# Performance work log

Hardware: AMD Instinct MI355X
Metric: run time of the kernel (lower is better)

Reference implementation:

```python
import jax, jax.numpy as jnp
import numpy as np

EPS = 1e-4  # LayerNorm epsilon from module


def layer_norm(x):
    # torch: (x - mean) / (std + eps), std unbiased (ddof=1), no affine
    mean = jnp.mean(x, axis=-1, keepdims=True)
    std = jnp.sqrt(jnp.var(x, axis=-1, ddof=1, keepdims=True))
    return (x - mean) / (std + EPS)


def setup_inputs() -> dict:
    key = jax.random.key(0)
    ks = jax.random.split(key, 9)
    B, S, D, H, QK = 2, 2048, 1024, 16, 64
    E = D // H  # per-head value/output dim
    scale = 0.02
    x = jax.random.normal(ks[0], (B, S, D), dtype=jnp.float32)
    # stacked per-head projection weights, Linear as x @ W + b
    Wq = jax.random.normal(ks[1], (H, D, QK), dtype=jnp.float32) * scale
    bq = jax.random.normal(ks[2], (H, QK), dtype=jnp.float32) * scale
    Wk = jax.random.normal(ks[3], (H, D, QK), dtype=jnp.float32) * scale
    bk = jax.random.normal(ks[4], (H, QK), dtype=jnp.float32) * scale
    Wv = jax.random.normal(ks[5], (H, D, E), dtype=jnp.float32) * scale
    bv = jax.random.normal(ks[6], (H, E), dtype=jnp.float32) * scale
    Wff = jax.random.normal(ks[7], (D, D), dtype=jnp.float32) * scale
    bff = jax.random.normal(ks[8], (D,), dtype=jnp.float32) * scale
    return {"x": x, "Wq": Wq, "bq": bq, "Wk": Wk, "bk": bk,
            "Wv": Wv, "bv": bv, "Wff": Wff, "bff": bff}


def reference(x, Wq, bq, Wk, bk, Wv, bv, Wff, bff):
    B, S, D = x.shape
    # all heads at once (vectorized over the Python per-head loop)
    Q = jnp.einsum('bsd,hdq->bhsq', x, Wq) + bq[None, :, None, :]
    K = jnp.einsum('bsd,hdq->bhsq', x, Wk) + bk[None, :, None, :]
    V = jnp.einsum('bsd,hde->bhse', x, Wv) + bv[None, :, None, :]
    scores = jnp.einsum('bhsq,bhtq->bhst', Q, K)  # [B,H,S,S]
    # masked_fill on tril(..., diagonal=-1): strictly-lower entries -> -inf
    mask = jnp.tril(jnp.ones((S, S), dtype=bool), k=-1)
    scores = jnp.where(mask[None, None], -jnp.inf, scores)
    # non-standard softmax axis: dim=-2 (over rows s, not keys t)
    attn = jax.nn.softmax(scores, axis=-2)
    heads = jnp.einsum('bhst,bhte->bhse', attn, V)  # [B,H,S,E]
    H, E = heads.shape[1], heads.shape[3]
    combined = heads.transpose(0, 2, 1, 3).reshape(B, S, H * E)  # concat heads
    x = layer_norm(x + combined)
    x = x + (x @ Wff + bff)
    return layer_norm(x)
```

## Files before the change

### kernel.cpp

```cpp
#include <hip/hip_runtime.h>
#include <hip/hip_bf16.h>
#include <math.h>

typedef unsigned short u16;
typedef __attribute__((ext_vector_type(8))) short short8;
typedef __attribute__((ext_vector_type(4))) short short4v;
typedef __attribute__((ext_vector_type(4))) float f32x4;

constexpr int B  = 2;
constexpr int S  = 2048;
constexpr int D  = 1024;
constexpr int H  = 16;
constexpr int DK = 64;
constexpr int BS = B * S;

__device__ __forceinline__ u16 f2b(float f) {
    __hip_bfloat16 h = __float2bfloat16(f);
    return *reinterpret_cast<u16*>(&h);
}
__device__ __forceinline__ float b2f(short s) {
    unsigned int u = ((unsigned int)(u16)s) << 16;
    return __builtin_bit_cast(float, u);
}

#define MFMA16(a, b, c) __builtin_amdgcn_mfma_f32_16x16x32_bf16((a), (b), (c), 0, 0, 0)

__global__ __launch_bounds__(256) void convert_x(const float* __restrict__ src,
                                                 u16* __restrict__ dst)
{
    size_t i = ((size_t)blockIdx.x * 256 + threadIdx.x) * 8;
    f32x4 a = *reinterpret_cast<const f32x4*>(src + i);
    f32x4 b = *reinterpret_cast<const f32x4*>(src + i + 4);
    short8 o;
    o[0] = (short)f2b(a[0]); o[1] = (short)f2b(a[1]);
    o[2] = (short)f2b(a[2]); o[3] = (short)f2b(a[3]);
    o[4] = (short)f2b(b[0]); o[5] = (short)f2b(b[1]);
    o[6] = (short)f2b(b[2]); o[7] = (short)f2b(b[3]);
    *reinterpret_cast<short8*>(dst + i) = o;
}

__global__ __launch_bounds__(256) void tconv(const float* __restrict__ src,
                                             u16* __restrict__ dst, int R, int C)
{
    const int bb = blockIdx.z;
    src += (size_t)bb * R * C;
    dst += (size_t)bb * R * C;
    const int c0 = blockIdx.x * 64, r0 = blockIdx.y * 64;
    __shared__ float Ts[64][65];
    const int tid = threadIdx.x;
    #pragma unroll
    for (int i = 0; i < 4; ++i) {
        int idx = i * 1024 + tid * 4;
        int r = idx >> 6, c = idx & 63;
        f32x4 v = *reinterpret_cast<const f32x4*>(&src[(size_t)(r0 + r) * C + c0 + c]);
        Ts[r][c] = v[0]; Ts[r][c + 1] = v[1]; Ts[r][c + 2] = v[2]; Ts[r][c + 3] = v[3];
    }
    __syncthreads();
    #pragma unroll
    for (int i = 0; i < 4; ++i) {
        int cc = i * 16 + (tid >> 4);
        int rr = (tid & 15) * 4;
        short4v pk;
        pk[0] = (short)f2b(Ts[rr][cc]);     pk[1] = (short)f2b(Ts[rr + 1][cc]);
        pk[2] = (short)f2b(Ts[rr + 2][cc]); pk[3] = (short)f2b(Ts[rr + 3][cc]);
        *reinterpret_cast<short4v*>(&dst[(size_t)(c0 + cc) * R + r0 + rr]) = pk;
    }
}

__global__ __launch_bounds__(256) void qkv_gemm(
    const u16* __restrict__ xb, const u16* __restrict__ WT,
    const float* __restrict__ bq, const float* __restrict__ bk, const float* __restrict__ bv,
    u16* __restrict__ Qw, u16* __restrict__ Kw, u16* __restrict__ Vtw)
{
    const int id   = blockIdx.x;
    const int xcd  = id & 7;
    const int j    = id >> 3;
    const int nblk = xcd * 3 + j % 3;
    const int mblk = j / 3;
    const int m0 = mblk * 128, n0 = nblk * 128;
    const int sel = n0 >> 10;
    const float* bias = sel == 0 ? bq : sel == 1 ? bk : bv;

    __shared__ u16 SM[2][128][64];

    const int tid = threadIdx.x;
    const int w = tid >> 6, ln = tid & 15, hi = (tid & 63) >> 4;
    const int wm = w >> 1, wn = w & 1;

    char* pa_ = (char*)&SM[0][0][0];
    char* pb_ = (char*)&SM[1][0][0];
    auto swz = [](int r, int cb) { return r * 128 + (cb ^ ((r & 7) << 4)); };

    f32x4 acc[4][4];
    #pragma unroll
    for (int m = 0; m < 4; ++m)
        #pragma unroll
        for (int n = 0; n < 4; ++n) acc[m][n] = f32x4{0.f, 0.f, 0.f, 0.f};

    short8 ra[4], rb[4];
    auto stageLoad = [&](int k0) {
        #pragma unroll
        for (int c = 0; c < 4; ++c) {
            int idx = c * 256 + tid, r = idx >> 3, col = (idx & 7) * 8;
            ra[c] = *reinterpret_cast<const short8*>(&xb[(size_t)(m0 + r) * D + k0 + col]);
            rb[c] = *reinterpret_cast<const short8*>(&WT[(size_t)(n0 + r) * D + k0 + col]);
        }
    };
    auto stageWrite = [&]() {
        #pragma unroll
        for (int c = 0; c < 4; ++c) {
            int idx = c * 256 + tid, r = idx >> 3, cb = (idx & 7) * 16;
            *reinterpret_cast<short8*>(pa_ + swz(r, cb)) = ra[c];
            *reinterpret_cast<short8*>(pb_ + swz(r, cb)) = rb[c];
        }
    };

    stageLoad(0);
    stageWrite();
    __syncthreads();

    for (int it = 0; it < 16; ++it) {
        const bool nxt = (it + 1 < 16);
        if (nxt) stageLoad((it + 1) * 64);
        #pragma unroll
        for (int ks = 0; ks < 2; ++ks) {
            short8 af[4], bf[4];
            #pragma unroll
            for (int m = 0; m < 4; ++m)
                af[m] = *reinterpret_cast<const short8*>(
                    pa_ + swz(wm * 64 + m * 16 + ln, ks * 64 + hi * 16));
            #pragma unroll
            for (int n = 0; n < 4; ++n)
                bf[n] = *reinterpret_cast<const short8*>(
                    pb_ + swz(wn * 64 + n * 16 + ln, ks * 64 + hi * 16));
            #pragma unroll
            for (int m = 0; m < 4; ++m)
                #pragma unroll
                for (int n = 0; n < 4; ++n)
                    acc[m][n] = MFMA16(af[m], bf[n], acc[m][n]);
        }
        __syncthreads();
        if (nxt) {
            stageWrite();
            __syncthreads();
        }
    }

    float bias4[4];
    #pragma unroll
    for (int n = 0; n < 4; ++n)
        bias4[n] = bias[(n0 & 1023) + wn * 64 + n * 16 + ln];

    char* eb = pa_;
    const int bidx  = m0 >> 11;
    const int sbase = m0 & 2047;
    const int h0    = (n0 & 1023) >> 6;

    if (sel < 2) {
        #pragma unroll
        for (int m = 0; m < 4; ++m)
            #pragma unroll
            for (int n = 0; n < 4; ++n)
                #pragma unroll
                for (int r = 0; r < 4; ++r) {
                    int row = wm * 64 + m * 16 + hi * 4 + r;
                    int col = wn * 64 + n * 16 + ln;
                    *reinterpret_cast<u16*>(eb + row * 256 + ((col * 2) ^ ((row & 7) << 4))) =
                        f2b(acc[m][n][r] + bias4[n]);
                }
        __syncthreads();
        u16* dst0 = sel == 0 ? Qw : Kw;
        #pragma unroll
        for (int c = 0; c < 8; ++c) {
            int idx = c * 256 + tid;
            int row = idx >> 4, g = idx & 15;
            short8 v = *reinterpret_cast<const short8*>(
                eb + row * 256 + ((g * 16) ^ ((row & 7) << 4)));
            int h = h0 + (g >> 3), j0 = (g & 7) * 8;
            *reinterpret_cast<short8*>(
                &dst0[((size_t)(bidx * H + h) * S + sbase + row) * DK + j0]) = v;
        }
    } else {
        #pragma unroll
        for (int m = 0; m < 4; ++m)
            #pragma unroll
            for (int n = 0; n < 4; ++n)
                #pragma unroll
                for (int r = 0; r < 4; ++r) {
                    int row = wm * 64 + m * 16 + hi * 4 + r;
                    int col = wn * 64 + n * 16 + ln;
                    *reinterpret_cast<u16*>(eb + col * 256 + ((row * 2) ^ ((col & 7) << 4))) =
                        f2b(acc[m][n][r] + bias4[n]);
                }
        __syncthreads();
        #pragma unroll
        for (int c = 0; c < 8; ++c) {
            int idx = c * 256 + tid;
            int e = idx >> 4, g = idx & 15;
            short8 v = *reinterpret_cast<const short8*>(
                eb + e * 256 + ((g * 16) ^ ((e & 7) << 4)));
            int h = h0 + (e >> 6), ein = e & 63;
            *reinterpret_cast<short8*>(
                &Vtw[((size_t)(bidx * H + h) * DK + ein) * S + sbase + g * 8]) = v;
        }
    }
}

__global__ __launch_bounds__(256) void col_stats(
    const u16* __restrict__ Qw, const u16* __restrict__ Kw,
    u16* __restrict__ Vtw)
{
    const int id = blockIdx.x;
    const int bh = (id & 7) * 4 + ((id >> 3) & 3);
    const int t0 = (31 - (id >> 5)) * 64;
    const u16* Qh = Qw + (size_t)bh * S * DK;
    const u16* Kh = Kw + (size_t)bh * S * DK;
    u16* Vh = Vtw + (size_t)bh * DK * S;

    __shared__ u16 Qs[2][64][64];
    __shared__ float zbuf[64];

    const int tid = threadIdx.x;
    const int w = tid >> 6, ln = tid & 15, hi = (tid & 63) >> 4;
    const int e0 = tid >> 3, sc = tid & 7;

    char* qb0 = (char*)&Qs[0][0][0];
    char* qb1 = (char*)&Qs[1][0][0];
    auto swz = [](int row, int colb) { return (row * 128 + colb) ^ ((row & 7) << 4); };

    short8 ak[2];
    #pragma unroll
    for (int ks = 0; ks < 2; ++ks)
        ak[ks] = *reinterpret_cast<const short8*>(
            &Kh[(size_t)(t0 + w * 16 + ln) * DK + ks * 32 + hi * 8]);

    float zs[4] = {0.f, 0.f, 0.f, 0.f};

    {
        short8 a = *reinterpret_cast<const short8*>(&Qh[(size_t)e0 * DK + sc * 8]);
        short8 b = *reinterpret_cast<const short8*>(&Qh[(size_t)(e0 + 32) * DK + sc * 8]);
        *reinterpret_cast<short8*>(qb0 + swz(e0, sc * 16)) = a;
        *reinterpret_cast<short8*>(qb0 + swz(e0 + 32, sc * 16)) = b;
    }
    __syncthreads();

    int cur = 0;
    for (int s0b = 0; s0b <= t0; s0b += 64) {
        const bool nxt = (s0b + 64 <= t0);
        short8 nq0, nq1;
        if (nxt) {
            nq0 = *reinterpret_cast<const short8*>(&Qh[(size_t)(s0b + 64 + e0) * DK + sc * 8]);
            nq1 = *reinterpret_cast<const short8*>(&Qh[(size_t)(s0b + 96 + e0) * DK + sc * 8]);
        }
        char* qb = cur ? qb1 : qb0;
        f32x4 c[4];
        #pragma unroll
        for (int n = 0; n < 4; ++n) c[n] = f32x4{0.f, 0.f, 0.f, 0.f};
        #pragma unroll
        for (int ks = 0; ks < 2; ++ks)
            #pragma unroll
            for (int n = 0; n < 4; ++n) {
                short8 bqf = *reinterpret_cast<const short8*>(
                    qb + swz(n * 16 + ln, ks * 64 + hi * 16));
                c[n] = MFMA16(ak[ks], bqf, c[n]);
            }
        if (s0b == t0) {
            #pragma unroll
            for (int n = 0; n < 4; ++n)
                #pragma unroll
                for (int r = 0; r < 4; ++r)
                    if (s0b + n * 16 + ln > t0 + w * 16 + hi * 4 + r)
                        c[n][r] = -INFINITY;
        }
        #pragma unroll
        for (int n = 0; n < 4; ++n)
            #pragma unroll
            for (int r = 0; r < 4; ++r)
                zs[r] += __expf(c[n][r]);
        if (nxt) {
            char* qn = cur ? qb0 : qb1;
            *reinterpret_cast<short8*>(qn + swz(e0, sc * 16)) = nq0;
            *reinterpret_cast<short8*>(qn + swz(e0 + 32, sc * 16)) = nq1;
        }
        __syncthreads();
        cur ^= 1;
    }

    #pragma unroll
    for (int r = 0; r < 4; ++r) {
        #pragma unroll
        for (int msk = 1; msk < 16; msk <<= 1)
            zs[r] += __shfl_xor(zs[r], msk, 64);
    }
    if (ln == 0) {
        #pragma unroll
        for (int r = 0; r < 4; ++r)
            zbuf[w * 16 + hi * 4 + r] = 1.f / zs[r];
    }
    __syncthreads();

    float iz[8];
    #pragma unroll
    for (int j = 0; j < 8; ++j) iz[j] = zbuf[sc * 8 + j];
    #pragma unroll
    for (int pass = 0; pass < 2; ++pass) {
        int e = e0 + 32 * pass;
        u16* vp = &Vh[(size_t)e * S + t0 + sc * 8];
        short8 v = *reinterpret_cast<short8*>(vp);
        short8 o;
        #pragma unroll
        for (int j = 0; j < 8; ++j) o[j] = (short)f2b(b2f(v[j]) * iz[j]);
        *reinterpret_cast<short8*>(vp) = o;
    }
}

__global__ __launch_bounds__(256) void attn_pv(
    const u16* __restrict__ Qw, const u16* __restrict__ Kw, const u16* __restrict__ Vtw,
    float* __restrict__ combined)
{
    const int id = blockIdx.x;
    const int bh = (id & 7) * 4 + ((id >> 3) & 3);
    const int s0 = (id >> 5) * 64;
    const int bidx = bh >> 4, h = bh & 15;
    const u16* Qh = Qw + (size_t)bh * S * DK;
    const u16* Kh = Kw + (size_t)bh * S * DK;
    const u16* Vh = Vtw + (size_t)bh * DK * S;

    __shared__ u16 Vs[2][64][64];
    __shared__ u16 Ps[64][72];

    const int tid = threadIdx.x;
    const int w = tid >> 6, ln = tid & 15, hi = (tid & 63) >> 4;
    const int e0 = tid >> 3, sc = tid & 7;

    char* vb0 = (char*)&Vs[0][0][0];
    char* vb1 = (char*)&Vs[1][0][0];
    auto swz = [](int row, int colb) { return (row * 128 + colb) ^ ((row & 7) << 4); };

    short8 bq[4][2];
    #pragma unroll
    for (int n = 0; n < 4; ++n)
        #pragma unroll
        for (int ks = 0; ks < 2; ++ks)
            bq[n][ks] = *reinterpret_cast<const short8*>(
                &Qh[(size_t)(s0 + n * 16 + ln) * DK + ks * 32 + hi * 8]);

    f32x4 acc[4];
    #pragma unroll
    for (int n = 0; n < 4; ++n) acc[n] = f32x4{0.f, 0.f, 0.f, 0.f};

    {
        short8 a = *reinterpret_cast<const short8*>(&Vh[(size_t)e0 * S + s0 + sc * 8]);
        short8 b = *reinterpret_cast<const short8*>(&Vh[(size_t)(e0 + 32) * S + s0 + sc * 8]);
        *reinterpret_cast<short8*>(vb0 + swz(e0, sc * 16)) = a;
        *reinterpret_cast<short8*>(vb0 + swz(e0 + 32, sc * 16)) = b;
    }

    short8 akA[2], akB[2];
    auto loadK = [&](short8 (&ak)[2], int t1) {
        #pragma unroll
        for (int ks = 0; ks < 2; ++ks)
            ak[ks] = *reinterpret_cast<const short8*>(
                &Kh[(size_t)(t1 + w * 16 + ln) * DK + ks * 32 + hi * 8]);
    };

    loadK(akA, s0);
    __syncthreads();
    int cur = 0;

    auto tile = [&](short8 (&ak)[2], int t1) {
        const bool nxt = (t1 + 64 < S);
        short8 nv0, nv1;
        if (nxt) {
            nv0 = *reinterpret_cast<const short8*>(&Vh[(size_t)e0 * S + t1 + 64 + sc * 8]);
            nv1 = *reinterpret_cast<const short8*>(&Vh[(size_t)(e0 + 32) * S + t1 + 64 + sc * 8]);
        }

        f32x4 st[4];
        #pragma unroll
        for (int n = 0; n < 4; ++n) st[n] = f32x4{0.f, 0.f, 0.f, 0.f};
        #pragma unroll
        for (int ks = 0; ks < 2; ++ks)
            #pragma unroll
            for (int n = 0; n < 4; ++n)
                st[n] = MFMA16(ak[ks], bq[n][ks], st[n]);

        const bool diag = (t1 == s0);
        #pragma unroll
        for (int n = 0; n < 4; ++n) {
            short4v pk;
            #pragma unroll
            for (int r = 0; r < 4; ++r) {
                float p = __expf(st[n][r]);
                if (diag && (s0 + n * 16 + ln) > (t1 + w * 16 + hi * 4 + r)) p = 0.f;
                pk[r] = (short)f2b(p);
            }
            *reinterpret_cast<short4v*>(&Ps[n * 16 + ln][w * 16 + hi * 4]) = pk;
        }
        __syncthreads();

        char* vb = cur ? vb1 : vb0;
        short8 pa[2];
        #pragma unroll
        for (int ks = 0; ks < 2; ++ks)
            pa[ks] = *reinterpret_cast<const short8*>(&Ps[w * 16 + ln][ks * 32 + hi * 8]);
        #pragma unroll
        for (int ks = 0; ks < 2; ++ks)
            #pragma unroll
            for (int n = 0; n < 4; ++n) {
                short8 vv = *reinterpret_cast<const short8*>(
                    vb + swz(n * 16 + ln, ks * 64 + hi * 16));
                acc[n] = MFMA16(pa[ks], vv, acc[n]);
            }

        if (nxt) {
            char* vn = cur ? vb0 : vb1;
            *reinterpret_cast<short8*>(vn + swz(e0, sc * 16)) = nv0;
            *reinterpret_cast<short8*>(vn + swz(e0 + 32, sc * 16)) = nv1;
        }
        __syncthreads();
        cur ^= 1;
    };

    int t1 = s0;
    while (t1 < S) {
        if (t1 + 64 < S) loadK(akB, t1 + 64);
        tile(akA, t1);
        t1 += 64;
        if (t1 >= S) break;
        if (t1 + 64 < S) loadK(akA, t1 + 64);
        tile(akB, t1);
        t1 += 64;
    }

    #pragma unroll
    for (int n = 0; n < 4; ++n)
        #pragma unroll
        for (int r = 0; r < 4; ++r) {
            int s = s0 + w * 16 + hi * 4 + r;
            combined[((size_t)bidx * S + s) * D + h * DK + n * 16 + ln] = acc[n][r];
        }
}

__global__ __launch_bounds__(256) void add_ln(
    const float* __restrict__ a, const float* __restrict__ bsrc,
    float* __restrict__ out, u16* __restrict__ outb)
{
    const int row = blockIdx.x;
    const int tid = threadIdx.x;
    const size_t base = (size_t)row * D;

    float v[4];
    float sum = 0.f;
    #pragma unroll
    for (int i = 0; i < 4; ++i) {
        int c = tid + i * 256;
        float t = a[base + c];
        if (bsrc) t += bsrc[base + c];
        v[i] = t;
        sum += t;
    }

    __shared__ float red[8];
    #pragma unroll
    for (int o = 32; o > 0; o >>= 1) sum += __shfl_down(sum, o, 64);
    const int lane = tid & 63, w = tid >> 6;
    if (lane == 0) red[w] = sum;
    __syncthreads();
    const float mean = (red[0] + red[1] + red[2] + red[3]) * (1.f / D);

    float s2 = 0.f;
    #pragma unroll
    for (int i = 0; i < 4; ++i) { float d2 = v[i] - mean; s2 += d2 * d2; }
    #pragma unroll
    for (int o = 32; o > 0; o >>= 1) s2 += __shfl_down(s2, o, 64);
    if (lane == 0) red[4 + w] = s2;
    __syncthreads();
    const float var = (red[4] + red[5] + red[6] + red[7]) * (1.f / (D - 1));
    const float scale = 1.f / (sqrtf(var) + 1e-4f);

    #pragma unroll
    for (int i = 0; i < 4; ++i) {
        int c = tid + i * 256;
        float o = (v[i] - mean) * scale;
        out[base + c] = o;
        if (outb) outb[base + c] = f2b(o);
    }
}

__global__ __launch_bounds__(256) void ffn(
    const float* __restrict__ x1, const u16* __restrict__ x1b,
    const u16* __restrict__ WffT, const float* __restrict__ bff,
    float* __restrict__ x2)
{
    const int id = blockIdx.x;
    const int m0 = ((id & 7) * 4 + ((id >> 3) & 3)) * 128;
    const int n0 = (id >> 5) * 128;
    __shared__ u16 Xs[128][72];
    __shared__ u16 Ws[128][72];
    const int tid = threadIdx.x;
    const int w = tid >> 6, ln = tid & 15, hi = (tid & 63) >> 4;
    const int wm = w >> 1, wn = w & 1;

    f32x4 acc[4][4];
    #pragma unroll
    for (int m = 0; m < 4; ++m)
        #pragma unroll
        for (int n = 0; n < 4; ++n) acc[m][n] = f32x4{0.f, 0.f, 0.f, 0.f};

    for (int k0 = 0; k0 < D; k0 += 64) {
        #pragma unroll
        for (int i = 0; i < 4; ++i) {
            int ch = i * 256 + tid;
            int r = ch >> 3, c = (ch & 7) * 8;
            *reinterpret_cast<short8*>(&Xs[r][c]) =
                *reinterpret_cast<const short8*>(&x1b[(size_t)(m0 + r) * D + k0 + c]);
            *reinterpret_cast<short8*>(&Ws[r][c]) =
                *reinterpret_cast<const short8*>(&WffT[(size_t)(n0 + r) * D + k0 + c]);
        }
        __syncthreads();
        #pragma unroll
        for (int ks = 0; ks < 2; ++ks) {
            short8 a[4], bb[4];
            #pragma unroll
            for (int m = 0; m < 4; ++m)
                a[m] = *reinterpret_cast<const short8*>(&Xs[wm * 64 + m * 16 + ln][ks * 32 + hi * 8]);
            #pragma unroll
            for (int n = 0; n < 4; ++n)
                bb[n] = *reinterpret_cast<const short8*>(&Ws[wn * 64 + n * 16 + ln][ks * 32 + hi * 8]);
            #pragma unroll
            for (int m = 0; m < 4; ++m)
                #pragma unroll
                for (int n = 0; n < 4; ++n)
                    acc[m][n] = MFMA16(a[m], bb[n], acc[m][n]);
        }
        __syncthreads();
    }

    float bf4[4];
    #pragma unroll
    for (int n = 0; n < 4; ++n) bf4[n] = bff[n0 + wn * 64 + n * 16 + ln];

    #pragma unroll
    for (int m = 0; m < 4; ++m)
        #pragma unroll
        for (int n = 0; n < 4; ++n)
            #pragma unroll
            for (int r = 0; r < 4; ++r) {
                int row = m0 + wm * 64 + m * 16 + hi * 4 + r;
                int col = n0 + wn * 64 + n * 16 + ln;
                size_t idx = (size_t)row * D + col;
                x2[idx] = x1[idx] + acc[m][n][r] + bf4[n];
            }
}

extern "C" void kernel_launch(void* const* d_in, const int* in_sizes, int n_in,
                              void* d_out, int out_size, void* d_ws, size_t ws_size,
                              hipStream_t stream)
{
    const float* x   = (const float*)d_in[0];
    const float* Wq  = (const float*)d_in[1];
    const float* bq  = (const float*)d_in[2];
    const float* Wk  = (const float*)d_in[3];
    const float* bk  = (const float*)d_in[4];
    const float* Wv  = (const float*)d_in[5];
    const float* bv  = (const float*)d_in[6];
    const float* Wff = (const float*)d_in[7];
    const float* bff = (const float*)d_in[8];
    float* out = (float*)d_out;

    const size_t NX = (size_t)BS * D;
    char* p = (char*)d_ws;
    auto alloc = [&](size_t bytes) { char* r = p; p += bytes; return r; };

    u16* xb    = (u16*)alloc(NX * 2);
    u16* WT    = (u16*)alloc((size_t)3 * H * DK * D * 2);
    u16* WffT  = (u16*)alloc((size_t)D * D * 2);
    u16* Qw    = (u16*)alloc(NX * 2);
    u16* Kw    = (u16*)alloc(NX * 2);
    u16* Vtw   = (u16*)alloc(NX * 2);
    float* combined = (float*)alloc(NX * 4);
    float* x1       = (float*)alloc(NX * 4);
    u16*   x1b = xb;
    float* x2  = (float*)Qw;

    convert_x<<<dim3(NX / 2048), 256, 0, stream>>>(x, xb);
    tconv<<<dim3(1, 16, 16), 256, 0, stream>>>(Wq, WT, D, DK);
    tconv<<<dim3(1, 16, 16), 256, 0, stream>>>(Wk, WT + (size_t)H * DK * D, D, DK);
    tconv<<<dim3(1, 16, 16), 256, 0, stream>>>(Wv, WT + (size_t)2 * H * DK * D, D, DK);
    tconv<<<dim3(16, 16, 1), 256, 0, stream>>>(Wff, WffT, D, D);

    qkv_gemm<<<dim3(768), 256, 0, stream>>>(
        xb, WT, bq, bk, bv, Qw, Kw, Vtw);

    col_stats<<<dim3(1024), 256, 0, stream>>>(Qw, Kw, Vtw);

    attn_pv<<<dim3(1024), 256, 0, stream>>>(Qw, Kw, Vtw, combined);

    add_ln<<<BS, 256, 0, stream>>>(x, combined, x1, x1b);

    ffn<<<dim3(256), 256, 0, stream>>>(x1, x1b, WffT, bff, x2);

    add_ln<<<BS, 256, 0, stream>>>(x2, nullptr, out, nullptr);
}
```

Measured before the change: 157.5 us.

## Use direct global-to-LDS loads with double-buffered shared memory in GEMMs

Replaces the register-staged global loads in the QKV projection GEMM and the FFN GEMM with global_load_lds instructions that write 16-byte chunks straight into a double-buffered, XOR-swizzled LDS tile. The swizzle is applied on the global source column so the LDS layout matches the existing swizzled fragment reads. This removes the extra register round-trip and one barrier per k-step, and lets the next tile's loads overlap the current tile's MFMAs. The cost is twice the LDS per block, which may lower occupancy, and the code now relies on the direct-to-LDS load's per-wave contiguous write semantics being correct.

Result: faster. 151.7 us (-3.6%).

```diff
diff --git a/kernel.cpp b/kernel.cpp
--- a/kernel.cpp
+++ b/kernel.cpp
@@ -3,6 +3,7 @@
 #include <math.h>
 
 typedef unsigned short u16;
+typedef unsigned int u32;
 typedef __attribute__((ext_vector_type(8))) short short8;
 typedef __attribute__((ext_vector_type(4))) short short4v;
 typedef __attribute__((ext_vector_type(4))) float f32x4;
@@ -24,6 +25,12 @@
 }
 
 #define MFMA16(a, b, c) __builtin_amdgcn_mfma_f32_16x16x32_bf16((a), (b), (c), 0, 0, 0)
+
+__device__ __forceinline__ void gload16(const u16* g, u16* l) {
+    __builtin_amdgcn_global_load_lds(
+        (const __attribute__((address_space(1))) u32*)g,
+        (__attribute__((address_space(3))) u32*)l, 16, 0, 0);
+}
 
 __global__ __launch_bounds__(256) void convert_x(const float* __restrict__ src,
                                                  u16* __restrict__ dst)
@@ -81,14 +88,19 @@
     const int sel = n0 >> 10;
     const float* bias = sel == 0 ? bq : sel == 1 ? bk : bv;
 
-    __shared__ u16 SM[2][128][64];
+    __shared__ u16 SM[2][2][128][64];
 
     const int tid = threadIdx.x;
     const int w = tid >> 6, ln = tid & 15, hi = (tid & 63) >> 4;
     const int wm = w >> 1, wn = w & 1;
-
-    char* pa_ = (char*)&SM[0][0][0];
-    char* pb_ = (char*)&SM[1][0][0];
+    const int l  = tid & 63;
+    const int lr = l >> 3;
+    const int lc8 = ((l & 7) ^ lr) * 8;
+
+    char* sA0 = (char*)&SM[0][0][0][0];
+    char* sB0 = (char*)&SM[0][1][0][0];
+    char* sA1 = (char*)&SM[1][0][0][0];
+    char* sB1 = (char*)&SM[1][1][0][0];
     auto swz = [](int r, int cb) { return r * 128 + (cb ^ ((r & 7) << 4)); };
 
     f32x4 acc[4][4];
@@ -97,42 +109,35 @@
         #pragma unroll
         for (int n = 0; n < 4; ++n) acc[m][n] = f32x4{0.f, 0.f, 0.f, 0.f};
 
-    short8 ra[4], rb[4];
-    auto stageLoad = [&](int k0) {
+    auto stage = [&](char* sa, char* sb, int k0) {
         #pragma unroll
         for (int c = 0; c < 4; ++c) {
-            int idx = c * 256 + tid, r = idx >> 3, col = (idx & 7) * 8;
-            ra[c] = *reinterpret_cast<const short8*>(&xb[(size_t)(m0 + r) * D + k0 + col]);
-            rb[c] = *reinterpret_cast<const short8*>(&WT[(size_t)(n0 + r) * D + k0 + col]);
+            int rbase = w * 32 + c * 8;
+            int row = rbase + lr;
+            gload16(&xb[(size_t)(m0 + row) * D + k0 + lc8], (u16*)(sa + rbase * 128));
+            gload16(&WT[(size_t)(n0 + row) * D + k0 + lc8], (u16*)(sb + rbase * 128));
         }
     };
-    auto stageWrite = [&]() {
-        #pragma unroll
-        for (int c = 0; c < 4; ++c) {
-            int idx = c * 256 + tid, r = idx >> 3, cb = (idx & 7) * 16;
-            *reinterpret_cast<short8*>(pa_ + swz(r, cb)) = ra[c];
-            *reinterpret_cast<short8*>(pb_ + swz(r, cb)) = rb[c];
-        }
-    };
-
-    stageLoad(0);
-    stageWrite();
+
+    stage(sA0, sB0, 0);
     __syncthreads();
 
     for (int it = 0; it < 16; ++it) {
-        const bool nxt = (it + 1 < 16);
-        if (nxt) stageLoad((it + 1) * 64);
+        char* ac = (it & 1) ? sA1 : sA0;
+        char* bc = (it & 1) ? sB1 : sB0;
+        if (it + 1 < 16)
+            stage((it & 1) ? sA0 : sA1, (it & 1) ? sB0 : sB1, (it + 1) * 64);
         #pragma unroll
         for (int ks = 0; ks < 2; ++ks) {
             short8 af[4], bf[4];
             #pragma unroll
             for (int m = 0; m < 4; ++m)
                 af[m] = *reinterpret_cast<const short8*>(
-                    pa_ + swz(wm * 64 + m * 16 + ln, ks * 64 + hi * 16));
+                    ac + swz(wm * 64 + m * 16 + ln, ks * 64 + hi * 16));
             #pragma unroll
             for (int n = 0; n < 4; ++n)
                 bf[n] = *reinterpret_cast<const short8*>(
-                    pb_ + swz(wn * 64 + n * 16 + ln, ks * 64 + hi * 16));
+                    bc + swz(wn * 64 + n * 16 + ln, ks * 64 + hi * 16));
             #pragma unroll
             for (int m = 0; m < 4; ++m)
                 #pragma unroll
@@ -140,10 +145,6 @@
                     acc[m][n] = MFMA16(af[m], bf[n], acc[m][n]);
         }
         __syncthreads();
-        if (nxt) {
-            stageWrite();
-            __syncthreads();
-        }
     }
 
     float bias4[4];
@@ -151,7 +152,7 @@
     for (int n = 0; n < 4; ++n)
         bias4[n] = bias[(n0 & 1023) + wn * 64 + n * 16 + ln];
 
-    char* eb = pa_;
+    char* eb = sA0;
     const int bidx  = m0 >> 11;
     const int sbase = m0 & 2047;
     const int h0    = (n0 & 1023) >> 6;
@@ -496,11 +497,21 @@
     const int id = blockIdx.x;
     const int m0 = ((id & 7) * 4 + ((id >> 3) & 3)) * 128;
     const int n0 = (id >> 5) * 128;
-    __shared__ u16 Xs[128][72];
-    __shared__ u16 Ws[128][72];
+
+    __shared__ u16 SM[2][2][128][64];
+
     const int tid = threadIdx.x;
     const int w = tid >> 6, ln = tid & 15, hi = (tid & 63) >> 4;
     const int wm = w >> 1, wn = w & 1;
+    const int l  = tid & 63;
+    const int lr = l >> 3;
+    const int lc8 = ((l & 7) ^ lr) * 8;
+
+    char* sA0 = (char*)&SM[0][0][0][0];
+    char* sB0 = (char*)&SM[0][1][0][0];
+    char* sA1 = (char*)&SM[1][0][0][0];
+    char* sB1 = (char*)&SM[1][1][0][0];
+    auto swz = [](int r, int cb) { return r * 128 + (cb ^ ((r & 7) << 4)); };
 
     f32x4 acc[4][4];
     #pragma unroll
@@ -508,31 +519,40 @@
         #pragma unroll
         for (int n = 0; n < 4; ++n) acc[m][n] = f32x4{0.f, 0.f, 0.f, 0.f};
 
-    for (int k0 = 0; k0 < D; k0 += 64) {
-        #pragma unroll
-        for (int i = 0; i < 4; ++i) {
-            int ch = i * 256 + tid;
-            int r = ch >> 3, c = (ch & 7) * 8;
-            *reinterpret_cast<short8*>(&Xs[r][c]) =
-                *reinterpret_cast<const short8*>(&x1b[(size_t)(m0 + r) * D + k0 + c]);
-            *reinterpret_cast<short8*>(&Ws[r][c]) =
-                *reinterpret_cast<const short8*>(&WffT[(size_t)(n0 + r) * D + k0 + c]);
-        }
-        __syncthreads();
+    auto stage = [&](char* sa, char* sb, int k0) {
+        #pragma unroll
+        for (int c = 0; c < 4; ++c) {
+            int rbase = w * 32 + c * 8;
+            int row = rbase + lr;
+            gload16(&x1b[(size_t)(m0 + row) * D + k0 + lc8], (u16*)(sa + rbase * 128));
+            gload16(&WffT[(size_t)(n0 + row) * D + k0 + lc8], (u16*)(sb + rbase * 128));
+        }
+    };
+
+    stage(sA0, sB0, 0);
+    __syncthreads();
+
+    for (int it = 0; it < 16; ++it) {
+        char* ac = (it & 1) ? sA1 : sA0;
+        char* bc = (it & 1) ? sB1 : sB0;
+        if (it + 1 < 16)
+            stage((it & 1) ? sA0 : sA1, (it & 1) ? sB0 : sB1, (it + 1) * 64);
         #pragma unroll
         for (int ks = 0; ks < 2; ++ks) {
-            short8 a[4], bb[4];
+            short8 af[4], bf[4];
             #pragma unroll
             for (int m = 0; m < 4; ++m)
-                a[m] = *reinterpret_cast<const short8*>(&Xs[wm * 64 + m * 16 + ln][ks * 32 + hi * 8]);
+                af[m] = *reinterpret_cast<const short8*>(
+                    ac + swz(wm * 64 + m * 16 + ln, ks * 64 + hi * 16));
             #pragma unroll
             for (int n = 0; n < 4; ++n)
-                bb[n] = *reinterpret_cast<const short8*>(&Ws[wn * 64 + n * 16 + ln][ks * 32 + hi * 8]);
+                bf[n] = *reinterpret_cast<const short8*>(
+                    bc + swz(wn * 64 + n * 16 + ln, ks * 64 + hi * 16));
             #pragma unroll
             for (int m = 0; m < 4; ++m)
                 #pragma unroll
                 for (int n = 0; n < 4; ++n)
-                    acc[m][n] = MFMA16(a[m], bb[n], acc[m][n]);
+                    acc[m][n] = MFMA16(af[m], bf[n], acc[m][n]);
         }
         __syncthreads();
     }
```
